# Optimization experiments

Measured on AMD Instinct MI355X. Metric: run time of the kernel, lower is better.

The kernel has to match this reference:

```python
import jax, jax.numpy as jnp
import numpy as np


def setup_inputs() -> dict:
    key = jax.random.key(0)
    kq, kk, kv = jax.random.split(key, 3)
    B, S, D = 4, 4096, 64
    return {
        "q": jax.random.normal(kq, (B, S, D), dtype=jnp.float32),
        "k": jax.random.normal(kk, (B, S, D), dtype=jnp.float32),
        "v": jax.random.normal(kv, (B, S, D), dtype=jnp.float32),
    }


def reference(q, k, v):
    B, S, D = q.shape
    scale = 1.0 / jnp.sqrt(jnp.asarray(D, dtype=q.dtype))
    # (B, S, S) full score matrix, as in the naive torch implementation
    scores = jnp.einsum("bqd,bkd->bqk", q, k) * scale
    causal_mask = jnp.tril(jnp.ones((S, S), dtype=bool))  # True = keep
    scores = jnp.where(causal_mask, scores, -jnp.inf)
    attn = jax.nn.softmax(scores, axis=-1)
    return jnp.einsum("bqk,bkd->bqd", attn, v)
```

## Files before the change

### kernel.cpp

```cpp
#include <hip/hip_runtime.h>
#include <hip/hip_bf16.h>

typedef __bf16 bf16x8 __attribute__((ext_vector_type(8)));
typedef __bf16 bf16x4 __attribute__((ext_vector_type(4)));
typedef float  floatx4 __attribute__((ext_vector_type(4)));

#define SD 4096
#define DH 64
#define NB 4

__device__ __forceinline__ float exp2fast(float x) { return __builtin_amdgcn_exp2f(x); }

__device__ __forceinline__ unsigned pack_bf16_2(float a, float b) {
    union { __bf16 h[2]; unsigned u; } cvt;
    cvt.h[0] = (__bf16)a; cvt.h[1] = (__bf16)b;
    return cvt.u;
}

__device__ __forceinline__ void sync_all() {
    asm volatile("s_waitcnt vmcnt(0) lgkmcnt(0)\n\ts_barrier" ::: "memory");
}

__device__ __forceinline__ void load_lds16(const void* g, void* l) {
    __builtin_amdgcn_global_load_lds(
        (const __attribute__((address_space(1))) unsigned int*)g,
        (__attribute__((address_space(3))) unsigned int*)l, 16, 0, 0);
}

__device__ __forceinline__ int swz8(int g) {
    int row = g >> 3, ch = g & 7;
    return row * 64 + ((ch ^ (row & 7)) << 3);
}

__global__ __launch_bounds__(256) void prep_kernel(const float* __restrict__ k,
                                                   const float* __restrict__ v,
                                                   __bf16* __restrict__ kbs,
                                                   __bf16* __restrict__ vts) {
    __shared__ __bf16 tile[64][72];
    const int bid = blockIdx.x;
    const int tid = threadIdx.x;
    const long base = (long)bid * 4096;

    {
        const float* src = k + base + tid * 16;
        float4 f0 = *(const float4*)(src);
        float4 f1 = *(const float4*)(src + 4);
        float4 f2 = *(const float4*)(src + 8);
        float4 f3 = *(const float4*)(src + 12);
        bf16x8 c0, c1;
        c0[0]=(__bf16)f0.x; c0[1]=(__bf16)f0.y; c0[2]=(__bf16)f0.z; c0[3]=(__bf16)f0.w;
        c0[4]=(__bf16)f1.x; c0[5]=(__bf16)f1.y; c0[6]=(__bf16)f1.z; c0[7]=(__bf16)f1.w;
        c1[0]=(__bf16)f2.x; c1[1]=(__bf16)f2.y; c1[2]=(__bf16)f2.z; c1[3]=(__bf16)f2.w;
        c1[4]=(__bf16)f3.x; c1[5]=(__bf16)f3.y; c1[6]=(__bf16)f3.z; c1[7]=(__bf16)f3.w;
        __bf16* dst = kbs + base;
        *(bf16x8*)(dst + swz8(tid * 2))     = c0;
        *(bf16x8*)(dst + swz8(tid * 2 + 1)) = c1;
    }
    {
        int r = tid >> 2, ds0 = (tid & 3) * 16;
#pragma unroll
        for (int i = 0; i < 4; ++i) {
            float4 f = *(const float4*)(v + base + r * 64 + ds0 + i * 4);
            tile[ds0 + i*4 + 0][r] = (__bf16)f.x;
            tile[ds0 + i*4 + 1][r] = (__bf16)f.y;
            tile[ds0 + i*4 + 2][r] = (__bf16)f.z;
            tile[ds0 + i*4 + 3][r] = (__bf16)f.w;
        }
    }
    __syncthreads();
    {
        __bf16* dst = vts + base;
#pragma unroll
        for (int h = 0; h < 2; ++h) {
            int qc = tid * 2 + h;
            int d = qc >> 3, c8 = (qc & 7) * 8;
            bf16x8 o;
#pragma unroll
            for (int i = 0; i < 8; ++i) {
                int col = c8 + i;
                int key = ((col >> 5) * 2 + ((col >> 2) & 1)) * 16
                        + ((col >> 3) & 3) * 4 + (col & 3);
                o[i] = tile[d][key];
            }
            *(bf16x8*)(dst + swz8(qc)) = o;
        }
    }
}

__global__ __launch_bounds__(256, 4) void fa_kernel(const float* __restrict__ q,
                                                    const __bf16* __restrict__ kbs,
                                                    const __bf16* __restrict__ vts,
                                                    __bf16* __restrict__ opart,
                                                    float* __restrict__ lpart) {
    __shared__ __bf16 smem[2][8192];

    const int tid  = threadIdx.x;
    const int wave = tid >> 6;
    const int lane = tid & 63;
    const int c    = lane & 15;
    const int quad = lane >> 4;
    const int bid   = blockIdx.x;
    const int batch = bid & 3;
    const int pr    = (bid >> 2) & 31;
    const int qr    = bid >> 7;
    const float sc = 0.125f * 1.4426950408889634f;

    const long offB = (long)batch * SD * DH;

    const int sw   = c & 7;
    const int off0 = ((quad ^ sw) << 3);
    const int off1 = (((quad + 4) ^ sw) << 3);
    const int rowc = c * 64;

    const long tileB = (long)batch * 64;

    auto stage = [&](int kt, int bufi) {
        const char* gsrc = (wave < 2)
            ? (const char*)(kbs + (tileB + kt) * 4096) + wave * 4096
            : (const char*)(vts + (tileB + kt) * 4096) + (wave - 2) * 4096;
        char* ldst = (char*)(&smem[bufi][0]) + wave * 4096;
#pragma unroll
        for (int i = 0; i < 4; ++i)
            load_lds16(gsrc + i * 1024 + lane * 16, ldst + i * 1024);
    };

#pragma unroll 1
    for (int ph = 0; ph < 2; ++ph) {
        const int T = ph ? 63 - pr : pr;
        const int myq = T * 64 + wave * 16;
        const int qrow = myq + c;

        bf16x8 qf0, qf1;
        {
            const float* qp = q + offB + (long)(myq + c) * DH + quad * 8;
            float4 f0 = *(const float4*)(qp);
            float4 f1 = *(const float4*)(qp + 4);
            float4 f2 = *(const float4*)(qp + 32);
            float4 f3 = *(const float4*)(qp + 36);
            qf0[0]=(__bf16)(f0.x*sc); qf0[1]=(__bf16)(f0.y*sc); qf0[2]=(__bf16)(f0.z*sc); qf0[3]=(__bf16)(f0.w*sc);
            qf0[4]=(__bf16)(f1.x*sc); qf0[5]=(__bf16)(f1.y*sc); qf0[6]=(__bf16)(f1.z*sc); qf0[7]=(__bf16)(f1.w*sc);
            qf1[0]=(__bf16)(f2.x*sc); qf1[1]=(__bf16)(f2.y*sc); qf1[2]=(__bf16)(f2.z*sc); qf1[3]=(__bf16)(f2.w*sc);
            qf1[4]=(__bf16)(f3.x*sc); qf1[5]=(__bf16)(f3.y*sc); qf1[6]=(__bf16)(f3.z*sc); qf1[7]=(__bf16)(f3.w*sc);
        }

        floatx4 o0 = {0.f,0.f,0.f,0.f}, o1 = o0, o2 = o0, o3 = o0;
        float l = 0.0f;

        const int n = (T >= qr) ? ((T - qr) >> 3) + 1 : 0;

        sync_all();
        if (n > 0) stage(qr, 0);

#pragma unroll 1
        for (int j = 0; j < n; ++j) {
            const int kt = qr + 8 * j;
            sync_all();
            if (j + 1 < n) stage(kt + 8, (j + 1) & 1);

            const int kbase = kt * 64;
            if (kbase > myq + 15) continue;

            const __bf16* kbuf = &smem[j & 1][0];
            const __bf16* vbuf = kbuf + 4096;
            floatx4 sa[4];
#pragma unroll
            for (int t = 0; t < 4; ++t) {
                bf16x8 ka  = *(const bf16x8*)(kbuf + t * 1024 + rowc + off0);
                bf16x8 kb2 = *(const bf16x8*)(kbuf + t * 1024 + rowc + off1);
                floatx4 a = {0.f,0.f,0.f,0.f};
                a = __builtin_amdgcn_mfma_f32_16x16x32_bf16(ka,  qf0, a, 0, 0, 0);
                a = __builtin_amdgcn_mfma_f32_16x16x32_bf16(kb2, qf1, a, 0, 0, 0);
                sa[t] = a;
            }
            float pe[16];
            if (kbase + 63 > myq) {
#pragma unroll
                for (int t = 0; t < 4; ++t)
#pragma unroll
                    for (int r = 0; r < 4; ++r) {
                        int key = kbase + t*16 + quad*4 + r;
                        pe[t*4+r] = (key <= qrow) ? exp2fast(sa[t][r]) : 0.0f;
                    }
            } else {
#pragma unroll
                for (int t = 0; t < 4; ++t)
#pragma unroll
                    for (int r = 0; r < 4; ++r) pe[t*4+r] = exp2fast(sa[t][r]);
            }
            {
                float s8[8], s4v[4];
#pragma unroll
                for (int i = 0; i < 8; ++i) s8[i] = pe[i] + pe[i+8];
#pragma unroll
                for (int i = 0; i < 4; ++i) s4v[i] = s8[i] + s8[i+4];
                l += (s4v[0] + s4v[2]) + (s4v[1] + s4v[3]);
            }
#pragma unroll
            for (int s = 0; s < 2; ++s) {
                union { unsigned u[4]; bf16x8 f; } bp;
#pragma unroll
                for (int jj = 0; jj < 4; ++jj)
                    bp.u[jj] = pack_bf16_2(pe[8*s + 2*jj], pe[8*s + 2*jj + 1]);
                const int offs = s ? off1 : off0;
                bf16x8 v0 = *(const bf16x8*)(vbuf + 0*1024 + rowc + offs);
                bf16x8 v1 = *(const bf16x8*)(vbuf + 1*1024 + rowc + offs);
                bf16x8 v2 = *(const bf16x8*)(vbuf + 2*1024 + rowc + offs);
                bf16x8 v3 = *(const bf16x8*)(vbuf + 3*1024 + rowc + offs);
                o0 = __builtin_amdgcn_mfma_f32_16x16x32_bf16(v0, bp.f, o0, 0, 0, 0);
                o1 = __builtin_amdgcn_mfma_f32_16x16x32_bf16(v1, bp.f, o1, 0, 0, 0);
                o2 = __builtin_amdgcn_mfma_f32_16x16x32_bf16(v2, bp.f, o2, 0, 0, 0);
                o3 = __builtin_amdgcn_mfma_f32_16x16x32_bf16(v3, bp.f, o3, 0, 0, 0);
            }
        }

        l += __shfl_xor(l, 16);
        l += __shfl_xor(l, 32);

        __bf16* ob = opart + ((long)qr * NB + batch) * (long)(SD * DH) + (long)myq * DH;
        {
            floatx4 ov[4] = {o0, o1, o2, o3};
#pragma unroll
            for (int dt = 0; dt < 4; ++dt) {
                uint2 sO;
                sO.x = pack_bf16_2(ov[dt][0], ov[dt][1]);
                sO.y = pack_bf16_2(ov[dt][2], ov[dt][3]);
                *(uint2*)(ob + c * DH + dt*16 + quad*4) = sO;
            }
        }
        if (quad == 0)
            lpart[((long)qr * NB + batch) * SD + myq + c] = l;
    }
}

__global__ __launch_bounds__(256) void combine_kernel(const __bf16* __restrict__ opart,
                                                      const float* __restrict__ lpart,
                                                      float* __restrict__ out) {
    const long t    = (long)blockIdx.x * 256 + threadIdx.x;
    const long base = t * 4;
    const long qq   = base >> 6;
    float n0 = 0.f, n1 = 0.f, n2 = 0.f, n3 = 0.f, den = 0.f;
#pragma unroll
    for (int qr = 0; qr < 8; ++qr) {
        bf16x4 p = *(const bf16x4*)(opart + ((long)qr << 20) + base);
        n0 += (float)p[0]; n1 += (float)p[1]; n2 += (float)p[2]; n3 += (float)p[3];
        den += lpart[((long)qr << 14) + qq];
    }
    float inv = 1.0f / den;
    float4 o; o.x = n0 * inv; o.y = n1 * inv; o.z = n2 * inv; o.w = n3 * inv;
    *(float4*)(out + base) = o;
}

extern "C" void kernel_launch(void* const* d_in, const int* in_sizes, int n_in,
                              void* d_out, int out_size, void* d_ws, size_t ws_size,
                              hipStream_t stream) {
    const float* q = (const float*)d_in[0];
    const float* k = (const float*)d_in[1];
    const float* v = (const float*)d_in[2];
    float* out = (float*)d_out;
    __bf16* kbs   = (__bf16*)d_ws;
    __bf16* vts   = (__bf16*)((char*)d_ws + (2u << 20));
    __bf16* opart = (__bf16*)((char*)d_ws + (4u << 20));
    float*  lpart = (float*)((char*)d_ws + (20u << 20));
    prep_kernel<<<dim3(256), dim3(256), 0, stream>>>(k, v, kbs, vts);
    fa_kernel<<<dim3(1024), dim3(256), 0, stream>>>(q, kbs, vts, opart, lpart);
    combine_kernel<<<dim3(1024), dim3(256), 0, stream>>>(opart, lpart, out);
}
```

Measured before the change: 90.23 us.

## Skip empty partial writes, trim combine reads, hoist Q loads, add MFMA priority

The attention kernel now loads and converts both phases' Q fragments once before the phase loop, raises wave priority around the MFMA sections, and skips writing partial outputs for query-tile/split pairs that have no keys. The combine kernel processes 8 elements per thread on half the grid and reads only the splits that can hold nonzero partials for each query tile. Together these cut wasted global writes and reads in the split-K reduction and hide Q load latency, at the cost of extra registers for the second Q set.

```diff
diff --git a/kernel.cpp b/kernel.cpp
--- a/kernel.cpp
+++ b/kernel.cpp
@@ -124,24 +124,37 @@
             load_lds16(gsrc + i * 1024 + lane * 16, ldst + i * 1024);
     };
 
+    bf16x8 qA0, qA1, qB0, qB1;
+    {
+        const int T0 = pr, T1 = 63 - pr;
+        const float* qp0 = q + offB + (long)(T0 * 64 + wave * 16 + c) * DH + quad * 8;
+        const float* qp1 = q + offB + (long)(T1 * 64 + wave * 16 + c) * DH + quad * 8;
+        float4 a0 = *(const float4*)(qp0);
+        float4 a1 = *(const float4*)(qp0 + 4);
+        float4 a2 = *(const float4*)(qp0 + 32);
+        float4 a3 = *(const float4*)(qp0 + 36);
+        float4 b0 = *(const float4*)(qp1);
+        float4 b1 = *(const float4*)(qp1 + 4);
+        float4 b2 = *(const float4*)(qp1 + 32);
+        float4 b3 = *(const float4*)(qp1 + 36);
+        qA0[0]=(__bf16)(a0.x*sc); qA0[1]=(__bf16)(a0.y*sc); qA0[2]=(__bf16)(a0.z*sc); qA0[3]=(__bf16)(a0.w*sc);
+        qA0[4]=(__bf16)(a1.x*sc); qA0[5]=(__bf16)(a1.y*sc); qA0[6]=(__bf16)(a1.z*sc); qA0[7]=(__bf16)(a1.w*sc);
+        qA1[0]=(__bf16)(a2.x*sc); qA1[1]=(__bf16)(a2.y*sc); qA1[2]=(__bf16)(a2.z*sc); qA1[3]=(__bf16)(a2.w*sc);
+        qA1[4]=(__bf16)(a3.x*sc); qA1[5]=(__bf16)(a3.y*sc); qA1[6]=(__bf16)(a3.z*sc); qA1[7]=(__bf16)(a3.w*sc);
+        qB0[0]=(__bf16)(b0.x*sc); qB0[1]=(__bf16)(b0.y*sc); qB0[2]=(__bf16)(b0.z*sc); qB0[3]=(__bf16)(b0.w*sc);
+        qB0[4]=(__bf16)(b1.x*sc); qB0[5]=(__bf16)(b1.y*sc); qB0[6]=(__bf16)(b1.z*sc); qB0[7]=(__bf16)(b1.w*sc);
+        qB1[0]=(__bf16)(b2.x*sc); qB1[1]=(__bf16)(b2.y*sc); qB1[2]=(__bf16)(b2.z*sc); qB1[3]=(__bf16)(b2.w*sc);
+        qB1[4]=(__bf16)(b3.x*sc); qB1[5]=(__bf16)(b3.y*sc); qB1[6]=(__bf16)(b3.z*sc); qB1[7]=(__bf16)(b3.w*sc);
+    }
+
 #pragma unroll 1
     for (int ph = 0; ph < 2; ++ph) {
         const int T = ph ? 63 - pr : pr;
         const int myq = T * 64 + wave * 16;
         const int qrow = myq + c;
 
-        bf16x8 qf0, qf1;
-        {
-            const float* qp = q + offB + (long)(myq + c) * DH + quad * 8;
-            float4 f0 = *(const float4*)(qp);
-            float4 f1 = *(const float4*)(qp + 4);
-            float4 f2 = *(const float4*)(qp + 32);
-            float4 f3 = *(const float4*)(qp + 36);
-            qf0[0]=(__bf16)(f0.x*sc); qf0[1]=(__bf16)(f0.y*sc); qf0[2]=(__bf16)(f0.z*sc); qf0[3]=(__bf16)(f0.w*sc);
-            qf0[4]=(__bf16)(f1.x*sc); qf0[5]=(__bf16)(f1.y*sc); qf0[6]=(__bf16)(f1.z*sc); qf0[7]=(__bf16)(f1.w*sc);
-            qf1[0]=(__bf16)(f2.x*sc); qf1[1]=(__bf16)(f2.y*sc); qf1[2]=(__bf16)(f2.z*sc); qf1[3]=(__bf16)(f2.w*sc);
-            qf1[4]=(__bf16)(f3.x*sc); qf1[5]=(__bf16)(f3.y*sc); qf1[6]=(__bf16)(f3.z*sc); qf1[7]=(__bf16)(f3.w*sc);
-        }
+        const bf16x8 qf0 = ph ? qB0 : qA0;
+        const bf16x8 qf1 = ph ? qB1 : qA1;
 
         floatx4 o0 = {0.f,0.f,0.f,0.f}, o1 = o0, o2 = o0, o3 = o0;
         float l = 0.0f;
@@ -163,6 +176,7 @@
             const __bf16* kbuf = &smem[j & 1][0];
             const __bf16* vbuf = kbuf + 4096;
             floatx4 sa[4];
+            __builtin_amdgcn_s_setprio(1);
 #pragma unroll
             for (int t = 0; t < 4; ++t) {
                 bf16x8 ka  = *(const bf16x8*)(kbuf + t * 1024 + rowc + off0);
@@ -172,6 +186,7 @@
                 a = __builtin_amdgcn_mfma_f32_16x16x32_bf16(kb2, qf1, a, 0, 0, 0);
                 sa[t] = a;
             }
+            __builtin_amdgcn_s_setprio(0);
             float pe[16];
             if (kbase + 63 > myq) {
 #pragma unroll
@@ -195,6 +210,7 @@
                 for (int i = 0; i < 4; ++i) s4v[i] = s8[i] + s8[i+4];
                 l += (s4v[0] + s4v[2]) + (s4v[1] + s4v[3]);
             }
+            __builtin_amdgcn_s_setprio(1);
 #pragma unroll
             for (int s = 0; s < 2; ++s) {
                 union { unsigned u[4]; bf16x8 f; } bp;
@@ -211,43 +227,51 @@
                 o2 = __builtin_amdgcn_mfma_f32_16x16x32_bf16(v2, bp.f, o2, 0, 0, 0);
                 o3 = __builtin_amdgcn_mfma_f32_16x16x32_bf16(v3, bp.f, o3, 0, 0, 0);
             }
+            __builtin_amdgcn_s_setprio(0);
         }
 
         l += __shfl_xor(l, 16);
         l += __shfl_xor(l, 32);
 
-        __bf16* ob = opart + ((long)qr * NB + batch) * (long)(SD * DH) + (long)myq * DH;
-        {
-            floatx4 ov[4] = {o0, o1, o2, o3};
-#pragma unroll
-            for (int dt = 0; dt < 4; ++dt) {
-                uint2 sO;
-                sO.x = pack_bf16_2(ov[dt][0], ov[dt][1]);
-                sO.y = pack_bf16_2(ov[dt][2], ov[dt][3]);
-                *(uint2*)(ob + c * DH + dt*16 + quad*4) = sO;
-            }
-        }
-        if (quad == 0)
-            lpart[((long)qr * NB + batch) * SD + myq + c] = l;
+        if (n > 0) {
+            __bf16* ob = opart + ((long)qr * NB + batch) * (long)(SD * DH) + (long)myq * DH;
+            {
+                floatx4 ov[4] = {o0, o1, o2, o3};
+#pragma unroll
+                for (int dt = 0; dt < 4; ++dt) {
+                    uint2 sO;
+                    sO.x = pack_bf16_2(ov[dt][0], ov[dt][1]);
+                    sO.y = pack_bf16_2(ov[dt][2], ov[dt][3]);
+                    *(uint2*)(ob + c * DH + dt*16 + quad*4) = sO;
+                }
+            }
+            if (quad == 0)
+                lpart[((long)qr * NB + batch) * SD + myq + c] = l;
+        }
     }
 }
 
 __global__ __launch_bounds__(256) void combine_kernel(const __bf16* __restrict__ opart,
                                                       const float* __restrict__ lpart,
                                                       float* __restrict__ out) {
-    const long t    = (long)blockIdx.x * 256 + threadIdx.x;
-    const long base = t * 4;
-    const long qq   = base >> 6;
-    float n0 = 0.f, n1 = 0.f, n2 = 0.f, n3 = 0.f, den = 0.f;
-#pragma unroll
-    for (int qr = 0; qr < 8; ++qr) {
-        bf16x4 p = *(const bf16x4*)(opart + ((long)qr << 20) + base);
-        n0 += (float)p[0]; n1 += (float)p[1]; n2 += (float)p[2]; n3 += (float)p[3];
+    const long t     = (long)blockIdx.x * 256 + threadIdx.x;
+    const long base8 = t * 8;
+    const long qq    = base8 >> 6;
+    const int  T     = ((int)(qq & (SD - 1))) >> 6;
+    const int  nqr   = (T < 7 ? T : 7) + 1;
+    float a0=0.f,a1=0.f,a2=0.f,a3=0.f,a4=0.f,a5=0.f,a6=0.f,a7=0.f, den=0.f;
+    for (int qr = 0; qr < nqr; ++qr) {
+        bf16x8 p = *(const bf16x8*)(opart + ((long)qr << 20) + base8);
+        a0 += (float)p[0]; a1 += (float)p[1]; a2 += (float)p[2]; a3 += (float)p[3];
+        a4 += (float)p[4]; a5 += (float)p[5]; a6 += (float)p[6]; a7 += (float)p[7];
         den += lpart[((long)qr << 14) + qq];
     }
-    float inv = 1.0f / den;
-    float4 o; o.x = n0 * inv; o.y = n1 * inv; o.z = n2 * inv; o.w = n3 * inv;
-    *(float4*)(out + base) = o;
+    const float inv = 1.0f / den;
+    float4 o0, o1;
+    o0.x = a0*inv; o0.y = a1*inv; o0.z = a2*inv; o0.w = a3*inv;
+    o1.x = a4*inv; o1.y = a5*inv; o1.z = a6*inv; o1.w = a7*inv;
+    *(float4*)(out + base8)     = o0;
+    *(float4*)(out + base8 + 4) = o1;
 }
 
 extern "C" void kernel_launch(void* const* d_in, const int* in_sizes, int n_in,
@@ -263,5 +287,5 @@
     float*  lpart = (float*)((char*)d_ws + (20u << 20));
     prep_kernel<<<dim3(256), dim3(256), 0, stream>>>(k, v, kbs, vts);
     fa_kernel<<<dim3(1024), dim3(256), 0, stream>>>(q, kbs, vts, opart, lpart);
-    combine_kernel<<<dim3(1024), dim3(256), 0, stream>>>(opart, lpart, out);
-}
+    combine_kernel<<<dim3(512), dim3(256), 0, stream>>>(opart, lpart, out);
+}
```

Measured after the change: 88.42 us, median of 2. 2.0% less time.
